# Kernel optimization log

Hardware: AMD Instinct MI355X
Metric: run time of the kernel (lower is better)

Reference implementation:

```python
import jax, jax.numpy as jnp
import numpy as np

D_MODEL = 1024
N_HEADS = 16

def setup_inputs() -> dict:
    key = jax.random.key(0)
    ks = jax.random.split(key, 11)
    B, L, S, D = 2, 2048, 2048, D_MODEL
    s = 1.0 / np.sqrt(D)
    return {
        "Q": jax.random.normal(ks[0], (B, L, D), jnp.float32),
        "K": jax.random.normal(ks[1], (B, S, D), jnp.float32),
        "V": jax.random.normal(ks[2], (B, S, D), jnp.float32),
        "Wq": jax.random.normal(ks[3], (D, D), jnp.float32) * s,
        "bq": jnp.zeros((D,), jnp.float32),
        "Wk": jax.random.normal(ks[4], (D, D), jnp.float32) * s,
        "bk": jnp.zeros((D,), jnp.float32),
        "Wv": jax.random.normal(ks[5], (D, D), jnp.float32) * s,
        "bv": jnp.zeros((D,), jnp.float32),
        "We": jax.random.normal(ks[6], (D, D), jnp.float32) * s,
        "be": jnp.zeros((D,), jnp.float32),
    }

def reference(Q, K, V, Wq, bq, Wk, bk, Wv, bv, We, be):
    B, L, D = Q.shape
    S = K.shape[1]
    H = N_HEADS
    E = D // H
    # projections, split heads
    q = (Q @ Wq + bq).reshape(B, L, H, E)
    k = (K @ Wk + bk).reshape(B, S, H, E)
    v = (V @ Wv + bv).reshape(B, S, H, E)
    scale = 1.0 / np.sqrt(E)
    scores = jnp.einsum('blhe,bshe->bhls', q, k)  # [B,H,L,S]
    A = jax.nn.softmax(scale * scores, axis=-1)   # dropout is identity in eval
    out = jnp.einsum('bhls,bshd->blhd', A, v).reshape(B, L, H * E)
    return out @ We + be
```

## Files before the change

### kernel.cpp

```cpp
#include <hip/hip_runtime.h>
#include <hip/hip_bf16.h>
#include <stdint.h>

typedef __bf16 bf16_t;
typedef bf16_t bf16x8 __attribute__((ext_vector_type(8)));
typedef float  f32x4  __attribute__((ext_vector_type(4)));
typedef float  f32x16 __attribute__((ext_vector_type(16)));

#define GLOAD16(gp, lp) __builtin_amdgcn_global_load_lds( \
    (const __attribute__((address_space(1))) void*)(gp),  \
    (__attribute__((address_space(3))) void*)(lp), 16, 0, 0)

#define EXP2F(x) __builtin_amdgcn_exp2f(x)

__device__ inline uint32_t pack2(float lo, float hi) {
    union { bf16_t h[2]; uint32_t u; } x;
    x.h[0] = (bf16_t)lo; x.h[1] = (bf16_t)hi;
    return x.u;
}

__global__ __launch_bounds__(256) void wtrans_kernel(
    const float* __restrict__ Wq, const float* __restrict__ Wk,
    const float* __restrict__ Wv, const float* __restrict__ We,
    bf16_t* __restrict__ WqT, bf16_t* __restrict__ WkT,
    bf16_t* __restrict__ WvT, bf16_t* __restrict__ WeT)
{
    __shared__ bf16_t T[64][65];
    const float* W = (blockIdx.z == 0) ? Wq : (blockIdx.z == 1) ? Wk
                   : (blockIdx.z == 2) ? Wv : We;
    bf16_t* O = (blockIdx.z == 0) ? WqT : (blockIdx.z == 1) ? WkT
              : (blockIdx.z == 2) ? WvT : WeT;
    const int k0 = blockIdx.y * 64, n0 = blockIdx.x * 64;
    const int t = threadIdx.x;
    for (int i = 0; i < 16; ++i) {
        int flat = t + i * 256;
        int r = flat >> 6, c = flat & 63;
        T[r][c] = (bf16_t)W[(size_t)(k0 + r) * 1024 + n0 + c];
    }
    __syncthreads();
    for (int i = 0; i < 16; ++i) {
        int flat = t + i * 256;
        int n = flat >> 6, kk = flat & 63;
        O[(size_t)(n0 + n) * 1024 + k0 + kk] = T[kk][n];
    }
}

template<bool A_F32, bool BATCHED>
__global__ __launch_bounds__(256)
void gemm2_kernel(const void* __restrict__ A0, const void* __restrict__ A1,
                  const void* __restrict__ A2,
                  const bf16_t* __restrict__ B0, const bf16_t* __restrict__ B1,
                  const bf16_t* __restrict__ B2,
                  const float* __restrict__ b0, const float* __restrict__ b1,
                  const float* __restrict__ b2,
                  void* __restrict__ C0, void* __restrict__ C1,
                  void* __restrict__ C2)
{
    constexpr int M = 4096, K = 1024, N = 1024;
    __shared__ bf16_t As[128 * 64];
    __shared__ bf16_t Bs[128 * 64];

    const int msel = BATCHED ? blockIdx.y : 0;
    const void*   Av   = (msel == 0) ? A0 : (msel == 1) ? A1 : A2;
    const bf16_t* Bt   = (msel == 0) ? B0 : (msel == 1) ? B1 : B2;
    const float*  bias = (msel == 0) ? b0 : (msel == 1) ? b1 : b2;
    void*         Cv   = (msel == 0) ? C0 : (msel == 1) ? C1 : C2;
    const int omode = BATCHED ? ((msel == 2) ? 2 : 0) : 1;

    const int xcd = blockIdx.x & 7, idx = blockIdx.x >> 3;
    const int bm = (xcd << 2) | (idx >> 3), bn = idx & 7;
    const int row0 = bm * 128, col0 = bn * 128;
    const int t = threadIdx.x, w = t >> 6, l = t & 63;
    const int wr = w >> 1, wc = w & 1;

    f32x4 acc[4][4];
    #pragma unroll
    for (int i = 0; i < 4; ++i)
        #pragma unroll
        for (int j = 0; j < 4; ++j)
            #pragma unroll
            for (int c = 0; c < 4; ++c) acc[i][j][c] = 0.f;

    for (int k0 = 0; k0 < K; k0 += 64) {
        #pragma unroll
        for (int i = 0; i < 4; ++i) {
            int chunk = (w * 4 + i) * 64 + l;
            int r = chunk >> 3, c = chunk & 7;
            GLOAD16(Bt + (size_t)(col0 + r) * K + k0 + ((c ^ (r & 7)) * 8),
                    &Bs[(w * 4 + i) * 512]);
        }
        #pragma unroll
        for (int i = 0; i < 4; ++i) {
            int chunk = i * 256 + t;
            int r = chunk >> 3, c = chunk & 7;
            bf16x8 pv;
            if (A_F32) {
                const float* src = (const float*)Av + (size_t)(row0 + r) * K + k0 + c * 8;
                float4 v0 = *(const float4*)(src);
                float4 v1 = *(const float4*)(src + 4);
                pv[0] = (bf16_t)v0.x; pv[1] = (bf16_t)v0.y;
                pv[2] = (bf16_t)v0.z; pv[3] = (bf16_t)v0.w;
                pv[4] = (bf16_t)v1.x; pv[5] = (bf16_t)v1.y;
                pv[6] = (bf16_t)v1.z; pv[7] = (bf16_t)v1.w;
            } else {
                pv = *(const bf16x8*)((const bf16_t*)Av + (size_t)(row0 + r) * K + k0 + c * 8);
            }
            *(bf16x8*)&As[r * 64 + ((c ^ (r & 7)) * 8)] = pv;
        }
        __syncthreads();

        #pragma unroll
        for (int eks = 0; eks < 2; ++eks) {
            bf16x8 af[4], bfv[4];
            #pragma unroll
            for (int mi = 0; mi < 4; ++mi) {
                int row = wr * 64 + mi * 16 + (l & 15);
                int sl = (eks * 4 + (l >> 4)) ^ (row & 7);
                af[mi] = *(const bf16x8*)&As[row * 64 + sl * 8];
            }
            #pragma unroll
            for (int ni = 0; ni < 4; ++ni) {
                int row = wc * 64 + ni * 16 + (l & 15);
                int sl = (eks * 4 + (l >> 4)) ^ (row & 7);
                bfv[ni] = *(const bf16x8*)&Bs[row * 64 + sl * 8];
            }
            __builtin_amdgcn_s_setprio(1);
            #pragma unroll
            for (int mi = 0; mi < 4; ++mi)
                #pragma unroll
                for (int ni = 0; ni < 4; ++ni)
                    acc[mi][ni] = __builtin_amdgcn_mfma_f32_16x16x32_bf16(
                        af[mi], bfv[ni], acc[mi][ni], 0, 0, 0);
            __builtin_amdgcn_s_setprio(0);
        }
        __syncthreads();
    }

    #pragma unroll
    for (int mi = 0; mi < 4; ++mi)
        #pragma unroll
        for (int ni = 0; ni < 4; ++ni) {
            int col = col0 + wc * 64 + ni * 16 + (l & 15);
            float bv = bias[col];
            int rowb = row0 + wr * 64 + mi * 16 + (l >> 4) * 4;
            if (omode == 2) {
                union { bf16_t h[4]; uint64_t q; } pk;
                #pragma unroll
                for (int j = 0; j < 4; ++j)
                    pk.h[j] = (bf16_t)(acc[mi][ni][j] + bv);
                *(uint64_t*)((bf16_t*)Cv + (size_t)col * M + rowb) = pk.q;
            } else if (omode == 1) {
                #pragma unroll
                for (int j = 0; j < 4; ++j)
                    ((float*)Cv)[(size_t)(rowb + j) * N + col] = acc[mi][ni][j] + bv;
            } else {
                #pragma unroll
                for (int j = 0; j < 4; ++j)
                    ((bf16_t*)Cv)[(size_t)(rowb + j) * N + col] = (bf16_t)(acc[mi][ni][j] + bv);
            }
        }
}

__global__ __launch_bounds__(256)
void attn4_kernel(const bf16_t* __restrict__ qp, const bf16_t* __restrict__ kp,
                  const bf16_t* __restrict__ vT, bf16_t* __restrict__ o)
{
    __shared__ bf16_t Ks[2][4096];
    __shared__ bf16_t Vs[2][4096];
    const int qb = blockIdx.x, bh = blockIdx.y;
    const int b = bh >> 4, h = bh & 15;
    const int t = threadIdx.x, w = t >> 6, l = t & 63;
    const int ql = l & 31, hh = l >> 5;
    const float M0 = 8.0f * 1.44269504f;

    const bf16_t* kbase = kp + ((size_t)b * 2048) * 1024 + h * 64;
    const bf16_t* vbase = vT + ((size_t)h * 64) * 4096 + (size_t)b * 2048;
    const int q0 = qb * 128 + w * 32;

    bf16x8 qf[4];
    {
        const bf16_t* qrow = qp + ((size_t)b * 2048 + q0 + ql) * 1024 + h * 64;
        const float qs = 0.125f * 1.44269504f;
        #pragma unroll
        for (int eks = 0; eks < 4; ++eks) {
            bf16x8 v = *(const bf16x8*)(qrow + eks * 16 + hh * 8);
            #pragma unroll
            for (int j = 0; j < 8; ++j) v[j] = (bf16_t)((float)v[j] * qs);
            qf[eks] = v;
        }
    }

    f32x16 acc0, acc1;
    #pragma unroll
    for (int r = 0; r < 16; ++r) { acc0[r] = 0.f; acc1[r] = 0.f; }
    float lsum = 0.f;

    const int r0 = t >> 3, r1 = 32 + (t >> 3), g = t & 7;
    const int w0off = r0 * 64 + ((g ^ (r0 & 7)) * 8);
    const int w1off = r1 * 64 + ((g ^ (r1 & 7)) * 8);

    {
        bf16x8 a = *(const bf16x8*)(kbase + (size_t)r0 * 1024 + g * 8);
        bf16x8 c = *(const bf16x8*)(kbase + (size_t)r1 * 1024 + g * 8);
        bf16x8 d = *(const bf16x8*)(vbase + (size_t)r0 * 4096 + g * 8);
        bf16x8 e = *(const bf16x8*)(vbase + (size_t)r1 * 4096 + g * 8);
        *(bf16x8*)&Ks[0][w0off] = a;  *(bf16x8*)&Ks[0][w1off] = c;
        *(bf16x8*)&Vs[0][w0off] = d;  *(bf16x8*)&Vs[0][w1off] = e;
    }
    __syncthreads();

    int cur = 0;
    for (int tile = 0; tile < 32; ++tile) {
        bf16x8 kr0, kr1, vr0, vr1;
        const bool pf = (tile + 1 < 32);
        if (pf) {
            const int s1 = (tile + 1) * 64;
            kr0 = *(const bf16x8*)(kbase + (size_t)(s1 + r0) * 1024 + g * 8);
            kr1 = *(const bf16x8*)(kbase + (size_t)(s1 + r1) * 1024 + g * 8);
            vr0 = *(const bf16x8*)(vbase + (size_t)r0 * 4096 + s1 + g * 8);
            vr1 = *(const bf16x8*)(vbase + (size_t)r1 * 4096 + s1 + g * 8);
        }

        f32x16 sA, sB;
        #pragma unroll
        for (int r = 0; r < 16; ++r) { sA[r] = 0.f; sB[r] = 0.f; }
        __builtin_amdgcn_s_setprio(1);
        #pragma unroll
        for (int eks = 0; eks < 4; ++eks) {
            bf16x8 k0 = *(const bf16x8*)&Ks[cur][ql * 64 + (((2 * eks + hh) ^ (ql & 7)) * 8)];
            bf16x8 k1 = *(const bf16x8*)&Ks[cur][(32 + ql) * 64 + (((2 * eks + hh) ^ (ql & 7)) * 8)];
            sA = __builtin_amdgcn_mfma_f32_32x32x16_bf16(k0, qf[eks], sA, 0, 0, 0);
            sB = __builtin_amdgcn_mfma_f32_32x32x16_bf16(k1, qf[eks], sB, 0, 0, 0);
        }
        __builtin_amdgcn_s_setprio(0);

        uint32_t wA[8], wB[8];
        float rs = 0.f;
        #pragma unroll
        for (int i = 0; i < 8; ++i) {
            float p0 = EXP2F(sA[2 * i]     - M0);
            float p1 = EXP2F(sA[2 * i + 1] - M0);
            rs += p0 + p1;  wA[i] = pack2(p0, p1);
            float p2 = EXP2F(sB[2 * i]     - M0);
            float p3 = EXP2F(sB[2 * i + 1] - M0);
            rs += p2 + p3;  wB[i] = pack2(p2, p3);
        }
        rs += __shfl_xor(rs, 32);
        lsum += rs;

        #pragma unroll
        for (int ks = 0; ks < 4; ++ks) {
            const int base = (ks & 1) * 4;
            uint32_t a0 = (ks < 2) ? wA[base]     : wB[base];
            uint32_t a1 = (ks < 2) ? wA[base + 1] : wB[base + 1];
            uint32_t a2 = (ks < 2) ? wA[base + 2] : wB[base + 2];
            uint32_t a3 = (ks < 2) ? wA[base + 3] : wB[base + 3];
            uint32_t x0 = (uint32_t)__shfl_xor((int)a0, 32);
            uint32_t x1 = (uint32_t)__shfl_xor((int)a1, 32);
            uint32_t x2 = (uint32_t)__shfl_xor((int)a2, 32);
            uint32_t x3 = (uint32_t)__shfl_xor((int)a3, 32);
            union { uint32_t u[4]; bf16x8 v; } pb;
            pb.u[0] = hh ? x2 : a0;
            pb.u[1] = hh ? x3 : a1;
            pb.u[2] = hh ? a2 : x0;
            pb.u[3] = hh ? a3 : x1;
            bf16x8 v0 = *(const bf16x8*)&Vs[cur][ql * 64 + (((2 * ks + hh) ^ (ql & 7)) * 8)];
            bf16x8 v1 = *(const bf16x8*)&Vs[cur][(32 + ql) * 64 + (((2 * ks + hh) ^ (ql & 7)) * 8)];
            __builtin_amdgcn_s_setprio(1);
            acc0 = __builtin_amdgcn_mfma_f32_32x32x16_bf16(v0, pb.v, acc0, 0, 0, 0);
            acc1 = __builtin_amdgcn_mfma_f32_32x32x16_bf16(v1, pb.v, acc1, 0, 0, 0);
            __builtin_amdgcn_s_setprio(0);
        }

        if (pf) {
            *(bf16x8*)&Ks[cur ^ 1][w0off] = kr0;
            *(bf16x8*)&Ks[cur ^ 1][w1off] = kr1;
            *(bf16x8*)&Vs[cur ^ 1][w0off] = vr0;
            *(bf16x8*)&Vs[cur ^ 1][w1off] = vr1;
        }
        __syncthreads();
        cur ^= 1;
    }

    bf16_t* sc = &Ks[0][0];
    const float inv = 1.0f / lsum;
    #pragma unroll
    for (int r = 0; r < 16; ++r) {
        int e = (r & 3) + 8 * (r >> 2) + 4 * hh;
        sc[w * 2048 + ql * 64 + (((e >> 3) ^ (ql & 7)) * 8) + (e & 7)] =
            (bf16_t)(acc0[r] * inv);
        int e2 = e + 32;
        sc[w * 2048 + ql * 64 + (((e2 >> 3) ^ (ql & 7)) * 8) + (e2 & 7)] =
            (bf16_t)(acc1[r] * inv);
    }
    __syncthreads();
    #pragma unroll
    for (int it = 0; it < 4; ++it) {
        int ci = it * 64 + l;
        int qr = ci >> 3, ec = ci & 7;
        bf16x8 ov = *(const bf16x8*)&sc[w * 2048 + qr * 64 + ((ec ^ (qr & 7)) * 8)];
        *(bf16x8*)(o + ((size_t)b * 2048 + q0 + qr) * 1024 + h * 64 + ec * 8) = ov;
    }
}

extern "C" void kernel_launch(void* const* d_in, const int* in_sizes, int n_in,
                              void* d_out, int out_size, void* d_ws, size_t ws_size,
                              hipStream_t stream)
{
    const float* Q  = (const float*)d_in[0];
    const float* K  = (const float*)d_in[1];
    const float* V  = (const float*)d_in[2];
    const float* Wq = (const float*)d_in[3];
    const float* bq = (const float*)d_in[4];
    const float* Wk = (const float*)d_in[5];
    const float* bk = (const float*)d_in[6];
    const float* Wv = (const float*)d_in[7];
    const float* bv = (const float*)d_in[8];
    const float* We = (const float*)d_in[9];
    const float* be = (const float*)d_in[10];
    float* out = (float*)d_out;

    bf16_t* ws = (bf16_t*)d_ws;
    bf16_t* WqT = ws;
    bf16_t* WkT = WqT + 1024 * 1024;
    bf16_t* WvT = WkT + 1024 * 1024;
    bf16_t* WeT = WvT + 1024 * 1024;
    bf16_t* qp  = WeT + 1024 * 1024;
    bf16_t* kp  = qp  + 4096 * 1024;
    bf16_t* vt  = kp  + 4096 * 1024;
    bf16_t* ao  = vt  + 4096 * 1024;

    dim3 blk(256);

    hipLaunchKernelGGL(wtrans_kernel, dim3(16, 16, 4), blk, 0, stream,
                       Wq, Wk, Wv, We, WqT, WkT, WvT, WeT);

    hipLaunchKernelGGL((gemm2_kernel<true, true>), dim3(256, 3), blk, 0, stream,
                       (const void*)Q, (const void*)K, (const void*)V,
                       WqT, WkT, WvT, bq, bk, bv,
                       (void*)qp, (void*)kp, (void*)vt);

    hipLaunchKernelGGL(attn4_kernel, dim3(16, 32), blk, 0, stream,
                       qp, kp, vt, ao);

    hipLaunchKernelGGL((gemm2_kernel<false, false>), dim3(256, 1), blk, 0, stream,
                       (const void*)ao, (const void*)nullptr, (const void*)nullptr,
                       WeT, (const bf16_t*)nullptr, (const bf16_t*)nullptr,
                       be, (const float*)nullptr, (const float*)nullptr,
                       (void*)out, (void*)nullptr, (void*)nullptr);
}
```

Measured before the change: 148.0 us.

## Pre-convert Q/K/V to bf16 and load GEMM A tiles via direct-to-LDS loads

Adds a separate conversion kernel that casts the fp32 Q, K, V inputs to bf16 in workspace. The projection and output GEMMs then load A tiles with global_load_lds directly into swizzled shared memory, as was already done for B, instead of loading through registers and converting in the loop. This removes register staging and conversion work from the GEMM main loop. In exchange it adds an extra kernel launch and a full fp32 read plus bf16 write and reread of the inputs, and it needs more workspace.

```diff
diff --git a/kernel.cpp b/kernel.cpp
--- a/kernel.cpp
+++ b/kernel.cpp
@@ -45,10 +45,29 @@
     }
 }
 
-template<bool A_F32, bool BATCHED>
 __global__ __launch_bounds__(256)
-void gemm2_kernel(const void* __restrict__ A0, const void* __restrict__ A1,
-                  const void* __restrict__ A2,
+void cvt_kernel(const float* __restrict__ X0, const float* __restrict__ X1,
+                const float* __restrict__ X2,
+                bf16_t* __restrict__ Y0, bf16_t* __restrict__ Y1,
+                bf16_t* __restrict__ Y2)
+{
+    const float* X = (blockIdx.y == 0) ? X0 : (blockIdx.y == 1) ? X1 : X2;
+    bf16_t*      Y = (blockIdx.y == 0) ? Y0 : (blockIdx.y == 1) ? Y1 : Y2;
+    size_t i0 = ((size_t)blockIdx.x * 256 + threadIdx.x) * 8;
+    float4 v0 = *(const float4*)(X + i0);
+    float4 v1 = *(const float4*)(X + i0 + 4);
+    bf16x8 pv;
+    pv[0] = (bf16_t)v0.x; pv[1] = (bf16_t)v0.y;
+    pv[2] = (bf16_t)v0.z; pv[3] = (bf16_t)v0.w;
+    pv[4] = (bf16_t)v1.x; pv[5] = (bf16_t)v1.y;
+    pv[6] = (bf16_t)v1.z; pv[7] = (bf16_t)v1.w;
+    *(bf16x8*)(Y + i0) = pv;
+}
+
+template<bool BATCHED>
+__global__ __launch_bounds__(256)
+void gemm3_kernel(const bf16_t* __restrict__ A0, const bf16_t* __restrict__ A1,
+                  const bf16_t* __restrict__ A2,
                   const bf16_t* __restrict__ B0, const bf16_t* __restrict__ B1,
                   const bf16_t* __restrict__ B2,
                   const float* __restrict__ b0, const float* __restrict__ b1,
@@ -61,7 +80,7 @@
     __shared__ bf16_t Bs[128 * 64];
 
     const int msel = BATCHED ? blockIdx.y : 0;
-    const void*   Av   = (msel == 0) ? A0 : (msel == 1) ? A1 : A2;
+    const bf16_t* Ab   = (msel == 0) ? A0 : (msel == 1) ? A1 : A2;
     const bf16_t* Bt   = (msel == 0) ? B0 : (msel == 1) ? B1 : B2;
     const float*  bias = (msel == 0) ? b0 : (msel == 1) ? b1 : b2;
     void*         Cv   = (msel == 0) ? C0 : (msel == 1) ? C1 : C2;
@@ -86,26 +105,9 @@
         for (int i = 0; i < 4; ++i) {
             int chunk = (w * 4 + i) * 64 + l;
             int r = chunk >> 3, c = chunk & 7;
-            GLOAD16(Bt + (size_t)(col0 + r) * K + k0 + ((c ^ (r & 7)) * 8),
-                    &Bs[(w * 4 + i) * 512]);
-        }
-        #pragma unroll
-        for (int i = 0; i < 4; ++i) {
-            int chunk = i * 256 + t;
-            int r = chunk >> 3, c = chunk & 7;
-            bf16x8 pv;
-            if (A_F32) {
-                const float* src = (const float*)Av + (size_t)(row0 + r) * K + k0 + c * 8;
-                float4 v0 = *(const float4*)(src);
-                float4 v1 = *(const float4*)(src + 4);
-                pv[0] = (bf16_t)v0.x; pv[1] = (bf16_t)v0.y;
-                pv[2] = (bf16_t)v0.z; pv[3] = (bf16_t)v0.w;
-                pv[4] = (bf16_t)v1.x; pv[5] = (bf16_t)v1.y;
-                pv[6] = (bf16_t)v1.z; pv[7] = (bf16_t)v1.w;
-            } else {
-                pv = *(const bf16x8*)((const bf16_t*)Av + (size_t)(row0 + r) * K + k0 + c * 8);
-            }
-            *(bf16x8*)&As[r * 64 + ((c ^ (r & 7)) * 8)] = pv;
+            int soff = (c ^ (r & 7)) * 8;
+            GLOAD16(Ab + (size_t)(row0 + r) * K + k0 + soff, &As[(w * 4 + i) * 512]);
+            GLOAD16(Bt + (size_t)(col0 + r) * K + k0 + soff, &Bs[(w * 4 + i) * 512]);
         }
         __syncthreads();
 
@@ -329,22 +331,27 @@
     bf16_t* kp  = qp  + 4096 * 1024;
     bf16_t* vt  = kp  + 4096 * 1024;
     bf16_t* ao  = vt  + 4096 * 1024;
+    bf16_t* Qb  = ao  + 4096 * 1024;
+    bf16_t* Kb  = Qb  + 4096 * 1024;
+    bf16_t* Vb  = Kb  + 4096 * 1024;
 
     dim3 blk(256);
 
     hipLaunchKernelGGL(wtrans_kernel, dim3(16, 16, 4), blk, 0, stream,
                        Wq, Wk, Wv, We, WqT, WkT, WvT, WeT);
 
-    hipLaunchKernelGGL((gemm2_kernel<true, true>), dim3(256, 3), blk, 0, stream,
-                       (const void*)Q, (const void*)K, (const void*)V,
-                       WqT, WkT, WvT, bq, bk, bv,
+    hipLaunchKernelGGL(cvt_kernel, dim3(2048, 3), blk, 0, stream,
+                       Q, K, V, Qb, Kb, Vb);
+
+    hipLaunchKernelGGL((gemm3_kernel<true>), dim3(256, 3), blk, 0, stream,
+                       Qb, Kb, Vb, WqT, WkT, WvT, bq, bk, bv,
                        (void*)qp, (void*)kp, (void*)vt);
 
     hipLaunchKernelGGL(attn4_kernel, dim3(16, 32), blk, 0, stream,
                        qp, kp, vt, ao);
 
-    hipLaunchKernelGGL((gemm2_kernel<false, false>), dim3(256, 1), blk, 0, stream,
-                       (const void*)ao, (const void*)nullptr, (const void*)nullptr,
+    hipLaunchKernelGGL((gemm3_kernel<false>), dim3(256, 1), blk, 0, stream,
+                       ao, (const bf16_t*)nullptr, (const bf16_t*)nullptr,
                        WeT, (const bf16_t*)nullptr, (const bf16_t*)nullptr,
                        be, (const float*)nullptr, (const float*)nullptr,
                        (void*)out, (void*)nullptr, (void*)nullptr);
```

Result: faster. 141.1 us (-4.7%).
